# Performance work log

Hardware: AMD Instinct MI355X
Metric: run time of the kernel (lower is better)

Reference implementation:

```python
import jax, jax.numpy as jnp
import numpy as np
from jax import lax

# model dims (must match init_kwargs)
NB, E, G0, G1 = 1, 64, 32, 256          # num_blocks, embed_dim, grid rows, grid cols
DM, DIN, DS, DC, DTR = 2048, 4096, 16, 4, 128  # d_model, d_inner, d_state, d_conv, dt_rank
PS, ST, KD = (2, 16), (2, 16), (31, 31)
B, C, T = 8, 64, 4096


def setup_inputs() -> dict:
    key = jax.random.key(0)
    ks = jax.random.split(key, 4)
    rng = np.random.default_rng(0)

    def w(*s, fan=None):
        fan = fan if fan is not None else s[-1]
        return jnp.asarray((rng.standard_normal(s) / np.sqrt(fan)).astype(np.float32))

    # mamba_ssm-style dt bias init: softplus(bias) ~ Uniform-log in [1e-3, 0.1]
    dt = np.exp(rng.uniform(size=(NB, 2, DIN)) * (np.log(0.1) - np.log(1e-3)) + np.log(1e-3))
    dt = np.clip(dt, 1e-4, None)
    bdt = jnp.asarray((dt + np.log(-np.expm1(-dt))).astype(np.float32))
    A_log = jnp.asarray(np.broadcast_to(np.log(np.arange(1, DS + 1, dtype=np.float32)), (NB, 2, DIN, DS)).copy())

    return {
        'x': jax.random.normal(ks[0], (B, C, T), dtype=jnp.float32),
        'mask': jax.random.uniform(ks[1], (B, C, T)) < 0.5,
        'proj_w': w(E, 1, PS[0], PS[1], fan=PS[0] * PS[1]),
        'proj_b': jnp.zeros((E,), jnp.float32),
        'pos_embed': 0.02 * jax.random.normal(ks[2], (1, G1, DM), dtype=jnp.float32),
        'in_proj_w': w(NB, 2, 2 * DIN, DM, fan=DM),
        'conv_w': w(NB, 2, DIN, DC, fan=DC),
        'conv_b': jnp.zeros((NB, 2, DIN), jnp.float32),
        'x_proj_w': w(NB, 2, DTR + 2 * DS, DIN, fan=DIN),
        'dt_proj_w': w(NB, 2, DIN, DTR, fan=DTR),
        'dt_proj_b': bdt,
        'A_log': A_log,
        'Dp': jnp.ones((NB, 2, DIN), jnp.float32),
        'out_proj_w': w(NB, 2, DM, DIN, fan=DIN),
        'ln_g': jnp.ones((NB, DM), jnp.float32),
        'ln_b': jnp.zeros((NB, DM), jnp.float32),
        'dec_conv_w': w(1, 1, KD[0], KD[1], fan=KD[0] * KD[1]),
        'convT_w': w(E, 1, PS[0], PS[1], fan=E),
        'convT_b': jnp.zeros((1,), jnp.float32),
    }


def _layernorm(x, g, b, eps=1e-5):
    m = jnp.mean(x, -1, keepdims=True)
    v = jnp.var(x, -1, keepdims=True)
    return (x - m) * lax.rsqrt(v + eps) * g + b


def _mamba(h, Win, Wc, bc, Wx, Wdt, bdt, Alog, Dp, Wout):
    # h: [B, L, DM]; faithful port of mamba_ssm Mamba (selective scan reference path)
    xz = jnp.einsum('bld,ed->ble', h, Win)               # [B, L, 2*DIN]
    xc, z = jnp.split(xz, 2, axis=-1)
    xc = xc.swapaxes(1, 2)                               # [B, DIN, L]
    xc = lax.conv_general_dilated(xc, Wc[:, None, :], (1,), ((DC - 1, 0),),
                                  dimension_numbers=('NCH', 'OIH', 'NCH'),
                                  feature_group_count=DIN) + bc[None, :, None]
    u = jax.nn.silu(xc).swapaxes(1, 2)                   # [B, L, DIN]
    x_dbl = jnp.einsum('bld,ed->ble', u, Wx)             # [B, L, DTR+2*DS]
    dt = jax.nn.softplus(jnp.einsum('blr,dr->bld', x_dbl[..., :DTR], Wdt) + bdt)
    Bm = x_dbl[..., DTR:DTR + DS]                        # [B, L, DS]
    Cm = x_dbl[..., DTR + DS:]                           # [B, L, DS]
    A = -jnp.exp(Alog)                                   # [DIN, DS]

    def step(hst, inp):
        dt_t, B_t, C_t, u_t = inp                        # [B,DIN],[B,DS],[B,DS],[B,DIN]
        dA = jnp.exp(dt_t[..., None] * A)                # [B, DIN, DS]
        hst = hst * dA + (dt_t * u_t)[..., None] * B_t[:, None, :]
        return hst, jnp.einsum('bds,bs->bd', hst, C_t)

    h0 = jnp.zeros((h.shape[0], DIN, DS), h.dtype)
    xs = (dt.swapaxes(0, 1), Bm.swapaxes(0, 1), Cm.swapaxes(0, 1), u.swapaxes(0, 1))
    _, ys = lax.scan(step, h0, xs)
    y = ys.swapaxes(0, 1) + u * Dp                       # [B, L, DIN]
    y = y * jax.nn.silu(z)
    return jnp.einsum('bld,ed->ble', y, Wout)            # [B, L, DM]


def _forward(x, mask, proj_w, proj_b, pos_embed, in_proj_w, conv_w, conv_b,
             x_proj_w, dt_proj_w, dt_proj_b, A_log, Dp, out_proj_w,
             ln_g, ln_b, dec_conv_w, convT_w, convT_b):
    xm = jnp.where(mask, 0.0, x)                         # x_masked[mask] = 0
    p = lax.conv_general_dilated(xm[:, None], proj_w, ST, 'VALID',
                                 dimension_numbers=('NCHW', 'OIHW', 'NCHW'))
    p = p + proj_b[None, :, None, None]                  # [B, E, G0, G1]
    h = p.reshape(p.shape[0], E * G0, G1).transpose(0, 2, 1) + pos_embed  # [B, G1, DM]
    for i in range(NB):
        a_f = (in_proj_w[i, 0], conv_w[i, 0], conv_b[i, 0], x_proj_w[i, 0], dt_proj_w[i, 0],
               dt_proj_b[i, 0], A_log[i, 0], Dp[i, 0], out_proj_w[i, 0])
        a_r = (in_proj_w[i, 1], conv_w[i, 1], conv_b[i, 1], x_proj_w[i, 1], dt_proj_w[i, 1],
               dt_proj_b[i, 1], A_log[i, 1], Dp[i, 1], out_proj_w[i, 1])
        o = _mamba(h, *a_f) + jnp.flip(_mamba(jnp.flip(h, 1), *a_r), 1)  # bidirectional add
        h = _layernorm(h + o, ln_g[i], ln_b[i])
    # Decoder
    d = lax.conv_general_dilated(h[:, None], dec_conv_w, (1, 1),
                                 (((KD[0] - 1) // 2,) * 2, ((KD[1] - 1) // 2,) * 2),
                                 dimension_numbers=('NCHW', 'OIHW', 'NCHW'))
    d = d[:, 0].transpose(0, 2, 1).reshape(-1, E, G0, G1)
    # ConvTranspose2d(E->1, k=PS, stride=ST) as lhs-dilated conv with flipped kernel
    wct = jnp.flip(convT_w, (2, 3)).swapaxes(0, 1)       # [1, E, kh, kw]
    rec = lax.conv_general_dilated(d, wct, (1, 1),
                                   ((PS[0] - 1, PS[0] - 1), (PS[1] - 1, PS[1] - 1)),
                                   lhs_dilation=ST,
                                   dimension_numbers=('NCHW', 'OIHW', 'NCHW'))
    rec = rec + convT_b[None, :, None, None]
    return rec[:, 0], x                                  # (x_reconstructed, x_original)


def reference(x, mask, proj_w, proj_b, pos_embed, in_proj_w, conv_w, conv_b,
              x_proj_w, dt_proj_w, dt_proj_b, A_log, Dp, out_proj_w,
              ln_g, ln_b, dec_conv_w, convT_w, convT_b):
    return _forward(x, mask, proj_w, proj_b, pos_embed, in_proj_w, conv_w, conv_b,
                    x_proj_w, dt_proj_w, dt_proj_b, A_log, Dp, out_proj_w,
                    ln_g, ln_b, dec_conv_w, convT_w, convT_b)
```

## Files before the change

kernel.cpp:

```cpp
#include <hip/hip_runtime.h>
#include <hip/hip_bf16.h>
#include <math.h>

typedef unsigned short u16;
typedef __attribute__((ext_vector_type(8))) short bf16x8;
typedef __attribute__((ext_vector_type(4))) float f32x4;

__device__ __forceinline__ float b2f(u16 v) {
  unsigned u = ((unsigned)v) << 16;
  return __builtin_bit_cast(float, u);
}
__device__ __forceinline__ u16 f2b(float f) {
  unsigned u = __builtin_bit_cast(unsigned, f);
  unsigned r = u + 0x7fffu + ((u >> 16) & 1u);
  return (u16)(r >> 16);
}
__device__ __forceinline__ void gload_lds16(const u16* g, u16* l) {
  __builtin_amdgcn_global_load_lds(
      (const __attribute__((address_space(1))) void*)g,
      (__attribute__((address_space(3))) void*)l, 16, 0, 0);
}

__global__ __launch_bounds__(256) void cvt_bf16_k(const float* __restrict__ s,
                                                  u16* __restrict__ d, int n4) {
  int i = blockIdx.x * 256 + threadIdx.x;
  if (i < n4) {
    float4 v = ((const float4*)s)[i];
    ushort4 o;
    o.x = f2b(v.x); o.y = f2b(v.y); o.z = f2b(v.z); o.w = f2b(v.w);
    ((ushort4*)d)[i] = o;
  }
}

__global__ __launch_bounds__(256) void toeplitz_k(
    const float* __restrict__ kw, u16* __restrict__ tb)
{
  int i = blockIdx.x * 256 + threadIdx.x;
  if (i >= 31744) return;
  int k = i & 31, n = (i >> 5) & 15, h = (i >> 9) & 1, ki = i >> 10;
  int t = h * 32 + k - n;
  float v = (t >= 0 && t <= 30) ? kw[ki * 31 + t] : 0.f;
  tb[i] = f2b(v);
}

__global__ __launch_bounds__(256) void patchify_k(
    const float* __restrict__ x, const int* __restrict__ mask,
    const float* __restrict__ pw, const float* __restrict__ pb,
    const float* __restrict__ pos, float* __restrict__ h, u16* __restrict__ hb)
{
  int g1 = blockIdx.x, b = blockIdx.y, tid = threadIdx.x;
  __shared__ float sX[64 * 17];
  __shared__ float sW[2048];
  for (int i = tid; i < 64 * 16; i += 256) {
    int r = i >> 4, c = i & 15;
    int gi = (b * 64 + r) * 4096 + g1 * 16 + c;
    sX[r * 17 + c] = mask[gi] ? 0.f : x[gi];
  }
  for (int i = tid; i < 2048; i += 256) sW[i] = pw[i];
  __syncthreads();
  for (int m = tid; m < 2048; m += 256) {
    int e = m >> 5, g0 = m & 31;
    float acc = pb[e];
    const float* w = &sW[e * 32];
#pragma unroll
    for (int kh = 0; kh < 2; ++kh)
#pragma unroll
      for (int kw = 0; kw < 16; ++kw)
        acc += sX[(2 * g0 + kh) * 17 + kw] * w[kh * 16 + kw];
    float v = acc + pos[g1 * 2048 + m];
    long o = ((long)b * 256 + g1) * 2048 + m;
    h[o] = v;
    hb[o] = f2b(v);
  }
}

__global__ __launch_bounds__(512, 2) void gemm256_k(
    const u16* __restrict__ A0,
    const u16* __restrict__ B0, long bStride,
    u16* __restrict__ C0, long cStride,
    const float* __restrict__ cw,
    const float* __restrict__ cb,
    u16* __restrict__ ub)
{
  constexpr int K = 2048, N = 8192, LDA = 2048;
  __shared__ __align__(16) u16 lds[67584];
  u16* As = lds;
  u16* Bs = lds + 32768;
  const int dir = blockIdx.z;
  const u16* A = A0;
  const u16* B = B0 + (long)dir * bStride;
  u16* C = C0 + (long)dir * cStride;
  const int flip = dir;

  const int tid = threadIdx.x;
  const int wave = tid >> 6, lane = tid & 63;
  const int wr = wave >> 2, wc = wave & 3;
  const int bm = blockIdx.y * 256, bn = blockIdx.x * 256;
  const int lr = lane & 15, lq = lane >> 4;

  f32x4 acc[8][4];
#pragma unroll
  for (int i = 0; i < 8; ++i)
#pragma unroll
    for (int j = 0; j < 4; ++j) acc[i][j] = (f32x4){0.f, 0.f, 0.f, 0.f};

  auto stage = [&](int buf, int kt) {
    int k0 = kt << 6;
#pragma unroll
    for (int hf = 0; hf < 2; ++hf)
#pragma unroll
      for (int j = 0; j < 2; ++j) {
        int g = j * 512 + tid;
        int rl = hf * 128 + (g >> 3);
        int gr = (g & 7) ^ ((g >> 3) & 7);
        int ar = flip ? (bm + 255 - rl) : (bm + rl);
        gload_lds16(A + (long)ar * LDA + k0 + gr * 8,
                    &As[buf * 16384 + hf * 8192 + g * 8]);
        gload_lds16(B + (long)(bn + rl) * K + k0 + gr * 8,
                    &Bs[buf * 16384 + hf * 8192 + g * 8]);
      }
  };

  const int nk = K >> 6;
  stage(0, 0);
  for (int kt = 0; kt < nk; ++kt) {
    __builtin_amdgcn_s_barrier();
    __builtin_amdgcn_sched_barrier(0);
    if (kt + 1 < nk) {
      stage((kt + 1) & 1, kt + 1);
      asm volatile("s_waitcnt vmcnt(16)" ::: "memory");
    } else {
      asm volatile("s_waitcnt vmcnt(0)" ::: "memory");
    }
    __builtin_amdgcn_sched_barrier(0);
    __builtin_amdgcn_s_barrier();
    __builtin_amdgcn_sched_barrier(0);
    const int buf = kt & 1;
#pragma unroll
    for (int h = 0; h < 2; ++h) {
      bf16x8 av[8], bv[4];
#pragma unroll
      for (int i = 0; i < 8; ++i) {
        int row = wr * 128 + i * 16 + lr;
        av[i] = *(const bf16x8*)
            &As[buf * 16384 + ((row * 64 + h * 32 + lq * 8) ^ ((row & 7) << 3))];
      }
#pragma unroll
      for (int j = 0; j < 4; ++j) {
        int row = wc * 64 + j * 16 + lr;
        bv[j] = *(const bf16x8*)
            &Bs[buf * 16384 + ((row * 64 + h * 32 + lq * 8) ^ ((row & 7) << 3))];
      }
      __builtin_amdgcn_s_setprio(1);
#pragma unroll
      for (int i = 0; i < 8; ++i)
#pragma unroll
        for (int j = 0; j < 4; ++j)
          acc[i][j] = __builtin_amdgcn_mfma_f32_16x16x32_bf16(
              av[i], bv[j], acc[i][j], 0, 0, 0);
      __builtin_amdgcn_s_setprio(0);
    }
  }

  if (bn < 4096) {
    __syncthreads();
    u16* tile = lds;
#pragma unroll
    for (int i = 0; i < 8; ++i) {
      int r0 = wr * 128 + i * 16 + lq * 4;
#pragma unroll
      for (int j = 0; j < 4; ++j) {
        int col = wc * 64 + j * 16 + lr;
        f32x4 v = acc[i][j];
#pragma unroll
        for (int r = 0; r < 4; ++r)
          tile[(r0 + r) * 264 + col] = f2b(v[r]);
      }
    }
    __syncthreads();
    const int rgrp = tid >> 5, c8 = tid & 31;
    const int d0 = bn + c8 * 8;
    float wv0[8], wv1[8], wv2[8], wv3[8], cbv[8];
#pragma unroll
    for (int e = 0; e < 8; ++e) {
      const float4 wq = *(const float4*)(cw + ((long)dir * 4096 + d0 + e) * 4);
      wv0[e] = wq.x; wv1[e] = wq.y; wv2[e] = wq.z; wv3[e] = wq.w;
      cbv[e] = cb[dir * 4096 + d0 + e];
    }
    const int l0 = rgrp * 16;
    float w0[8], w1[8], w2[8];
#pragma unroll
    for (int e = 0; e < 8; ++e) { w0[e] = 0.f; w1[e] = 0.f; w2[e] = 0.f; }
    if (rgrp > 0) {
      bf16x8 t0 = *(const bf16x8*)&tile[(l0 - 3) * 264 + c8 * 8];
      bf16x8 t1 = *(const bf16x8*)&tile[(l0 - 2) * 264 + c8 * 8];
      bf16x8 t2 = *(const bf16x8*)&tile[(l0 - 1) * 264 + c8 * 8];
#pragma unroll
      for (int e = 0; e < 8; ++e) {
        w0[e] = b2f((u16)t0[e]); w1[e] = b2f((u16)t1[e]); w2[e] = b2f((u16)t2[e]);
      }
    }
    long ubase = ((long)(dir * 8 + blockIdx.y) * 256 + l0) * 4096 + d0;
#pragma unroll
    for (int l = 0; l < 16; ++l) {
      bf16x8 t = *(const bf16x8*)&tile[(l0 + l) * 264 + c8 * 8];
      float cur[8];
#pragma unroll
      for (int e = 0; e < 8; ++e) cur[e] = b2f((u16)t[e]);
      bf16x8 ov;
#pragma unroll
      for (int e = 0; e < 8; ++e) {
        float a = cbv[e] + wv0[e] * w0[e] + wv1[e] * w1[e] + wv2[e] * w2[e] +
                  wv3[e] * cur[e];
        ov[e] = (short)f2b(a / (1.f + __expf(-a)));
      }
      *(bf16x8*)(ub + ubase + (long)l * 4096) = ov;
#pragma unroll
      for (int e = 0; e < 8; ++e) { w0[e] = w1[e]; w1[e] = w2[e]; w2[e] = cur[e]; }
    }
  } else {
#pragma unroll
    for (int i = 0; i < 8; ++i) {
      int r0 = bm + wr * 128 + i * 16 + lq * 4;
#pragma unroll
      for (int j = 0; j < 4; ++j) {
        int col = bn + wc * 64 + j * 16 + lr;
        f32x4 v = acc[i][j];
#pragma unroll
        for (int r = 0; r < 4; ++r)
          C[(long)(r0 + r) * N + col] = f2b(v[r]);
      }
    }
  }
}

template <int EPI, int F32OUT, int BFOUT>
__global__ __launch_bounds__(256) void mfma_gemm_k(
    const u16* __restrict__ A0, long aStride,
    const u16* __restrict__ B0, long bStride,
    float* __restrict__ C0, long cStride,
    u16* __restrict__ Cb0, long cbStride,
    const float* __restrict__ bias0, int biasStride,
    int N, int K, int lda, int flipDir1)
{
  __shared__ __align__(16) u16 As[2][4096];
  __shared__ __align__(16) u16 Bs[2][4096];
  const int dir = blockIdx.z;
  const u16* A = A0 + (long)dir * aStride;
  const u16* B = B0 + (long)dir * bStride;
  float* C = F32OUT ? (C0 + (long)dir * cStride) : nullptr;
  u16* Cb = BFOUT ? (Cb0 + (long)dir * cbStride) : nullptr;
  const float* bias = (EPI == 1) ? (bias0 + (long)dir * biasStride) : nullptr;
  const int flip = flipDir1 && (dir == 1);

  const int tid = threadIdx.x;
  const int wave = tid >> 6, lane = tid & 63;
  const int wr = wave >> 1, wc = wave & 1;
  const int bm = blockIdx.y * 128, bn = blockIdx.x * 128;
  const int lr = lane & 15, lq = lane >> 4;

  f32x4 acc[4][4];
#pragma unroll
  for (int i = 0; i < 4; ++i)
#pragma unroll
    for (int j = 0; j < 4; ++j) acc[i][j] = (f32x4){0.f, 0.f, 0.f, 0.f};

  const int nk = K >> 5;

  auto stage = [&](int buf, int k0) {
#pragma unroll
    for (int iss = 0; iss < 2; ++iss) {
      int ob = wave * 2048 + iss * 1024 + lane * 16;
      int row = ob >> 6, kb = (ob >> 4) & 3;
      int rg = bm + row;
      rg = flip ? ((rg & ~255) | (255 - (rg & 255))) : rg;
      gload_lds16(A + (long)rg * lda + k0 + kb * 8,
                  &As[buf][wave * 1024 + iss * 512]);
      int rb = bn + row; rb = (rb < N) ? rb : (N - 1);
      gload_lds16(B + (long)rb * K + k0 + kb * 8,
                  &Bs[buf][wave * 1024 + iss * 512]);
    }
  };

  stage(0, 0);
  for (int kt = 0; kt < nk; ++kt) {
    __syncthreads();
    if (kt + 1 < nk) stage((kt + 1) & 1, (kt + 1) << 5);
    const int buf = kt & 1;
    bf16x8 av[4], bv[4];
#pragma unroll
    for (int i = 0; i < 4; ++i)
      av[i] = *(const bf16x8*)&As[buf][(wr * 64 + i * 16 + lr) * 32 + lq * 8];
#pragma unroll
    for (int j = 0; j < 4; ++j)
      bv[j] = *(const bf16x8*)&Bs[buf][(wc * 64 + j * 16 + lr) * 32 + lq * 8];
#pragma unroll
    for (int i = 0; i < 4; ++i)
#pragma unroll
      for (int j = 0; j < 4; ++j)
        acc[i][j] = __builtin_amdgcn_mfma_f32_16x16x32_bf16(av[i], bv[j],
                                                            acc[i][j], 0, 0, 0);
  }

#pragma unroll
  for (int i = 0; i < 4; ++i) {
    int r0 = bm + wr * 64 + i * 16 + lq * 4;
#pragma unroll
    for (int j = 0; j < 4; ++j) {
      int col = bn + wc * 64 + j * 16 + lr;
      if (col < N) {
        f32x4 v = acc[i][j];
#pragma unroll
        for (int r = 0; r < 4; ++r) {
          float xv = v[r];
          if (EPI == 1) {
            xv += bias[col];
            xv = (xv > 20.f) ? xv : log1pf(expf(xv));
          }
          if (F32OUT) C[(long)(r0 + r) * N + col] = xv;
          if (BFOUT) Cb[(long)(r0 + r) * N + col] = f2b(xv);
        }
      }
    }
  }
}

__global__ __launch_bounds__(256) void xdbl_part_k(
    const u16* __restrict__ ubf, const u16* __restrict__ Wxbf,
    float* __restrict__ part)
{
  __shared__ __align__(16) u16 As[2][4096];
  __shared__ __align__(16) u16 Bs[2][4096];
  const int dir = blockIdx.z >> 2, split = blockIdx.z & 3;
  const u16* A = ubf + (long)dir * 2048 * 4096;
  const u16* B = Wxbf + (long)dir * 160 * 4096;
  float* C = part + (long)blockIdx.z * 327680;
  const int tid = threadIdx.x;
  const int wave = tid >> 6, lane = tid & 63;
  const int wr = wave >> 1, wc = wave & 1;
  const int bm = blockIdx.y * 128, bn = blockIdx.x * 128;
  const int lr = lane & 15, lq = lane >> 4;

  f32x4 acc[4][4];
#pragma unroll
  for (int i = 0; i < 4; ++i)
#pragma unroll
    for (int j = 0; j < 4; ++j) acc[i][j] = (f32x4){0.f, 0.f, 0.f, 0.f};

  auto stage = [&](int buf, int k0) {
#pragma unroll
    for (int iss = 0; iss < 2; ++iss) {
      int ob = wave * 2048 + iss * 1024 + lane * 16;
      int row = ob >> 6, kb = (ob >> 4) & 3;
      gload_lds16(A + (long)(bm + row) * 4096 + k0 + kb * 8,
                  &As[buf][wave * 1024 + iss * 512]);
      int rb = bn + row; rb = (rb < 160) ? rb : 159;
      gload_lds16(B + (long)rb * 4096 + k0 + kb * 8,
                  &Bs[buf][wave * 1024 + iss * 512]);
    }
  };

  const int kbase = split << 10;
  stage(0, kbase);
  for (int kt = 0; kt < 32; ++kt) {
    __syncthreads();
    if (kt + 1 < 32) stage((kt + 1) & 1, kbase + ((kt + 1) << 5));
    const int buf = kt & 1;
    bf16x8 av[4], bv[4];
#pragma unroll
    for (int i = 0; i < 4; ++i)
      av[i] = *(const bf16x8*)&As[buf][(wr * 64 + i * 16 + lr) * 32 + lq * 8];
#pragma unroll
    for (int j = 0; j < 4; ++j)
      bv[j] = *(const bf16x8*)&Bs[buf][(wc * 64 + j * 16 + lr) * 32 + lq * 8];
#pragma unroll
    for (int i = 0; i < 4; ++i)
#pragma unroll
      for (int j = 0; j < 4; ++j)
        acc[i][j] = __builtin_amdgcn_mfma_f32_16x16x32_bf16(av[i], bv[j],
                                                            acc[i][j], 0, 0, 0);
  }

#pragma unroll
  for (int i = 0; i < 4; ++i) {
    int r0 = bm + wr * 64 + i * 16 + lq * 4;
#pragma unroll
    for (int j = 0; j < 4; ++j) {
      int col = bn + wc * 64 + j * 16 + lr;
      if (col < 160) {
        f32x4 v = acc[i][j];
#pragma unroll
        for (int r = 0; r < 4; ++r)
          C[(long)(r0 + r) * 160 + col] = v[r];
      }
    }
  }
}

__global__ __launch_bounds__(256) void xdbl_reduce_k(
    const float* __restrict__ part, float* __restrict__ xdbl,
    u16* __restrict__ xdbl_bf)
{
  int i = blockIdx.x * 256 + threadIdx.x;
  if (i >= 655360) return;
  int dir = i / 327680, rem = i - dir * 327680;
  long pb = (long)dir * 4 * 327680 + rem;
  float s = part[pb] + part[pb + 327680] + part[pb + 2 * 327680] +
            part[pb + 3 * 327680];
  xdbl[i] = s;
  xdbl_bf[i] = f2b(s);
}

__global__ __launch_bounds__(256) void scan_a_k(
    const u16* __restrict__ dtbuf, const u16* __restrict__ ubuf,
    const float* __restrict__ xdbl, const float* __restrict__ A_log,
    const float* __restrict__ Dpv, u16* __restrict__ ypre,
    float* __restrict__ stend, float* __restrict__ dtsum)
{
  int blk = blockIdx.x;
  int dtile = blk & 15, c = (blk >> 4) & 7, b = (blk >> 7) & 7, dir = blk >> 10;
  int tid = threadIdx.x;
  int d = dtile * 256 + tid;
  int db = dir * 8 + b;

  __shared__ float sB[32][16], sC[32][16];
  long r160 = (long)db * 256 * 160;
  for (int i = tid; i < 1024; i += 256) {
    int l = i >> 5, s = i & 31;
    float v = xdbl[r160 + (long)(c * 32 + l) * 160 + 128 + s];
    if (s < 16) sB[l][s] = v; else sC[l][s - 16] = v;
  }
  __syncthreads();

  float A[16], st[16];
  const float4* ap = (const float4*)(A_log + ((long)dir * 4096 + d) * 16);
#pragma unroll
  for (int q = 0; q < 4; ++q) {
    float4 t = ap[q];
    A[q * 4 + 0] = -__expf(t.x); A[q * 4 + 1] = -__expf(t.y);
    A[q * 4 + 2] = -__expf(t.z); A[q * 4 + 3] = -__expf(t.w);
  }
#pragma unroll
  for (int s = 0; s < 16; ++s) st[s] = 0.f;
  float Dpd = Dpv[dir * 4096 + d];

  long base = (long)db * 256 * 4096 + (long)c * 32 * 4096 + d;
  float dts = 0.f;
  for (int i = 0; i < 32; ++i) {
    float dtv = b2f(dtbuf[base + (long)i * 4096]);
    float uv  = b2f(ubuf[base + (long)i * 4096]);
    dts += dtv;
    float du = dtv * uv;
    float y = 0.f;
#pragma unroll
    for (int s = 0; s < 16; ++s) {
      st[s] = st[s] * __expf(dtv * A[s]) + du * sB[i][s];
      y += st[s] * sC[i][s];
    }
    ypre[base + (long)i * 4096] = f2b(y + uv * Dpd);
  }
  long eb = ((long)(db * 8 + c) * 4096 + d) * 16;
  float4* ep = (float4*)(stend + eb);
#pragma unroll
  for (int q = 0; q < 4; ++q)
    ep[q] = make_float4(st[q * 4], st[q * 4 + 1], st[q * 4 + 2], st[q * 4 + 3]);
  dtsum[(long)(db * 8 + c) * 4096 + d] = dts;
}

__global__ __launch_bounds__(512) void scan_b_k(
    const u16* __restrict__ dtbuf, const u16* __restrict__ xzbf,
    const float* __restrict__ xdbl, const float* __restrict__ A_log,
    const float* __restrict__ stend, const float* __restrict__ dtsum,
    u16* __restrict__ ybuf)
{
  int blk = blockIdx.x;
  int dtile = blk & 63, b = (blk >> 6) & 7, dir = blk >> 9;
  int tid = threadIdx.x;
  int c = tid >> 6, dd = tid & 63;
  int d0 = dtile * 64, d = d0 + dd;
  int db = dir * 8 + b;

  __shared__ float sEnd[8][64][17];
  __shared__ float sT[8][64];
  __shared__ float sC[256][16];

  long eBase = (long)db * 8 * 65536;
  for (int i = tid; i < 8192; i += 512) {
    int cc = i >> 10, rem = i & 1023, dd2 = rem >> 4, s = rem & 15;
    sEnd[cc][dd2][s] = stend[eBase + (long)cc * 65536 + (long)(d0 + dd2) * 16 + s];
  }
  {
    int cc = tid >> 6, dd2 = tid & 63;
    sT[cc][dd2] = dtsum[(long)(db * 8 + cc) * 4096 + d0 + dd2];
  }
  long r160 = (long)db * 256 * 160;
  for (int i = tid; i < 4096; i += 512) {
    int l = i >> 4, s = i & 15;
    sC[l][s] = xdbl[r160 + (long)l * 160 + 144 + s];
  }
  __syncthreads();

  float A[16];
  const float4* ap = (const float4*)(A_log + ((long)dir * 4096 + d) * 16);
#pragma unroll
  for (int q = 0; q < 4; ++q) {
    float4 t = ap[q];
    A[q * 4 + 0] = -__expf(t.x); A[q * 4 + 1] = -__expf(t.y);
    A[q * 4 + 2] = -__expf(t.z); A[q * 4 + 3] = -__expf(t.w);
  }
  float g[16];
#pragma unroll
  for (int s = 0; s < 16; ++s) g[s] = 0.f;
  for (int j = 0; j < c; ++j) {
    float Tj = sT[j][dd];
#pragma unroll
    for (int s = 0; s < 16; ++s)
      g[s] = g[s] * __expf(A[s] * Tj) + sEnd[j][dd][s];
  }

  long base  = (long)db * 256 * 4096 + (long)c * 32 * 4096 + d;
  long zbase = (long)db * 256 * 8192 + (long)c * 32 * 8192 + 4096 + d;
  float cum = 0.f;
  if (c == 0) {
    for (int i = 0; i < 32; ++i) {
      float yp = b2f(ybuf[base + (long)i * 4096]);
      float zv = b2f(xzbf[zbase + (long)i * 8192]);
      float y = yp * (zv / (1.f + __expf(-zv)));
      ybuf[base + (long)i * 4096] = f2b(y);
    }
  } else {
    for (int i = 0; i < 32; ++i) {
      float dtv = b2f(dtbuf[base + (long)i * 4096]);
      cum += dtv;
      float yp = b2f(ybuf[base + (long)i * 4096]);
      float corr = 0.f;
      const int l = c * 32 + i;
#pragma unroll
      for (int s = 0; s < 16; ++s)
        corr += sC[l][s] * __expf(A[s] * cum) * g[s];
      float zv = b2f(xzbf[zbase + (long)i * 8192]);
      float y = (yp + corr) * (zv / (1.f + __expf(-zv)));
      ybuf[base + (long)i * 4096] = f2b(y);
    }
  }
}

__global__ __launch_bounds__(256) void add_ln_k(
    const float* __restrict__ h, const float* __restrict__ o0,
    const float* __restrict__ o1, const float* __restrict__ g,
    const float* __restrict__ bta, float* __restrict__ h2)
{
  int row = blockIdx.x;
  int b = row >> 8, l = row & 255;
  long base = (long)row * 2048;
  long base1 = ((long)b * 256 + (255 - l)) * 2048;
  int t8 = threadIdx.x * 8;
  float v[8];
  float4 x0 = *(const float4*)(h + base + t8);
  float4 x1 = *(const float4*)(h + base + t8 + 4);
  float4 a0 = *(const float4*)(o0 + base + t8);
  float4 a1 = *(const float4*)(o0 + base + t8 + 4);
  float4 c0 = *(const float4*)(o1 + base1 + t8);
  float4 c1 = *(const float4*)(o1 + base1 + t8 + 4);
  v[0] = x0.x + a0.x + c0.x; v[1] = x0.y + a0.y + c0.y;
  v[2] = x0.z + a0.z + c0.z; v[3] = x0.w + a0.w + c0.w;
  v[4] = x1.x + a1.x + c1.x; v[5] = x1.y + a1.y + c1.y;
  v[6] = x1.z + a1.z + c1.z; v[7] = x1.w + a1.w + c1.w;
  float s = 0.f, ss = 0.f;
#pragma unroll
  for (int j = 0; j < 8; ++j) { s += v[j]; ss += v[j] * v[j]; }
#pragma unroll
  for (int off = 32; off >= 1; off >>= 1) {
    s += __shfl_xor(s, off, 64);
    ss += __shfl_xor(ss, off, 64);
  }
  __shared__ float red[8];
  int wid = threadIdx.x >> 6, lane = threadIdx.x & 63;
  if (lane == 0) { red[wid] = s; red[wid + 4] = ss; }
  __syncthreads();
  if (threadIdx.x == 0) {
    red[0] = red[0] + red[1] + red[2] + red[3];
    red[4] = red[4] + red[5] + red[6] + red[7];
  }
  __syncthreads();
  float mean = red[0] * (1.f / 2048.f);
  float var = red[4] * (1.f / 2048.f) - mean * mean;
  float inv = rsqrtf(var + 1e-5f);
  float o[8];
#pragma unroll
  for (int j = 0; j < 8; ++j)
    o[j] = (v[j] - mean) * inv * g[t8 + j] + bta[t8 + j];
  *(float4*)(h2 + base + t8) = make_float4(o[0], o[1], o[2], o[3]);
  *(float4*)(h2 + base + t8 + 4) = make_float4(o[4], o[5], o[6], o[7]);
}

__global__ __launch_bounds__(256) void dec_conv31_k(
    const float* __restrict__ h2, const u16* __restrict__ tb,
    float* __restrict__ dc)
{
  __shared__ __align__(16) u16 sIn[94 * 120];
  const int b = blockIdx.z;
  const int l0 = blockIdx.y * 64;
  const int m0 = blockIdx.x * 64;
  const int tid = threadIdx.x;
  const float* src = h2 + (long)b * 256 * 2048;
  for (int i = tid; i < 94 * 112; i += 256) {
    int r = i / 112, c = i - r * 112;
    int gl = l0 + r - 15, gm = m0 + c - 15;
    float v = 0.f;
    if (gl >= 0 && gl < 256 && gm >= 0 && gm < 2048)
      v = src[(long)gl * 2048 + gm];
    sIn[r * 120 + c] = f2b(v);
  }
  __syncthreads();
  const int wave = tid >> 6, lane = tid & 63;
  const int lr = lane & 15, lq = lane >> 4;

  f32x4 acc[4];
#pragma unroll
  for (int s = 0; s < 4; ++s) acc[s] = (f32x4){0.f, 0.f, 0.f, 0.f};

#pragma unroll 1
  for (int ki = 0; ki < 31; ++ki) {
    const u16* arow = &sIn[(wave * 16 + lr + ki) * 120];
#pragma unroll
    for (int h = 0; h < 2; ++h) {
      bf16x8 bv = *(const bf16x8*)&tb[((ki * 2 + h) * 16 + lr) * 32 + lq * 8];
#pragma unroll
      for (int ms = 0; ms < 4; ++ms) {
        bf16x8 av = *(const bf16x8*)&arow[ms * 16 + h * 32 + lq * 8];
        acc[ms] = __builtin_amdgcn_mfma_f32_16x16x32_bf16(av, bv, acc[ms], 0, 0, 0);
      }
    }
  }
#pragma unroll
  for (int ms = 0; ms < 4; ++ms) {
    f32x4 v = acc[ms];
#pragma unroll
    for (int r = 0; r < 4; ++r)
      dc[((long)b * 256 + l0 + wave * 16 + lq * 4 + r) * 2048 + m0 + ms * 16 + lr]
          = v[r];
  }
}

__global__ __launch_bounds__(256) void convT_k(
    const float* __restrict__ dc, const float* __restrict__ w,
    const float* __restrict__ wb, float* __restrict__ out)
{
  int j = blockIdx.x, b = blockIdx.y;
  __shared__ float sD[2048];
  __shared__ float sW[2048];
  int tid = threadIdx.x;
  const float* drow = dc + ((long)b * 256 + j) * 2048;
  for (int i = tid; i < 2048; i += 256) { sD[i] = drow[i]; sW[i] = w[i]; }
  __syncthreads();
  float cb = wb[0];
  int owlo = tid & 15, ohbase = tid >> 4;
#pragma unroll
  for (int q = 0; q < 4; ++q) {
    int oh = ohbase + q * 16;
    int i = oh >> 1, a = oh & 1;
    float acc = cb;
#pragma unroll 8
    for (int e = 0; e < 64; ++e)
      acc += sD[e * 32 + i] * sW[e * 32 + a * 16 + owlo];
    out[((long)b * 64 + oh) * 4096 + j * 16 + owlo] = acc;
  }
}

extern "C" void kernel_launch(void* const* d_in, const int* in_sizes, int n_in,
                              void* d_out, int out_size, void* d_ws, size_t ws_size,
                              hipStream_t stream)
{
  const float* x      = (const float*)d_in[0];
  const int*   mask   = (const int*)d_in[1];
  const float* proj_w = (const float*)d_in[2];
  const float* proj_b = (const float*)d_in[3];
  const float* pos    = (const float*)d_in[4];
  const float* Wip    = (const float*)d_in[5];
  const float* convw  = (const float*)d_in[6];
  const float* convb  = (const float*)d_in[7];
  const float* Wx     = (const float*)d_in[8];
  const float* Wdt    = (const float*)d_in[9];
  const float* bdt    = (const float*)d_in[10];
  const float* Alog   = (const float*)d_in[11];
  const float* Dpv    = (const float*)d_in[12];
  const float* Wout   = (const float*)d_in[13];
  const float* lng    = (const float*)d_in[14];
  const float* lnb    = (const float*)d_in[15];
  const float* dkw    = (const float*)d_in[16];
  const float* ctw    = (const float*)d_in[17];
  const float* ctb    = (const float*)d_in[18];
  float* out = (float*)d_out;

  char* p = (char*)d_ws;
  u16*   xz_bf   = (u16*)p;
  float* ob      = (float*)p;
  p += 67108864;
  u16*   u_bf    = (u16*)p;
  float* dc      = (float*)p;
  p += 33554432;
  u16*   dt_bf   = (u16*)p; p += 67108864;
  float* xdbl    = (float*)p; p += 2621440;
  u16*   xdbl_bf = (u16*)p;  p += 1310720;
  float* h       = (float*)p; p += 16777216;
  u16*   h_bf    = (u16*)p;  p += 8388608;
  float* h2      = (float*)p; p += 16777216;
  u16*   y_bf    = (u16*)p;  p += 33554432;
  u16*   Wpool   = (u16*)p;  p += 67108864;
  u16*   Wx_bf   = (u16*)p;  p += 2621440;
  u16*   Wdt_bf  = (u16*)p;  p += 2097152;
  u16*   tb      = (u16*)p;  p += 65536;

  float* part   = (float*)(Wpool + 16777216);
  float* st_end = (float*)(Wpool + 16777216);
  float* dtsum  = h2;

  cvt_bf16_k<<<32768, 256, 0, stream>>>(Wip, Wpool, 8388608);
  cvt_bf16_k<<<1280, 256, 0, stream>>>(Wx, Wx_bf, 327680);
  cvt_bf16_k<<<1024, 256, 0, stream>>>(Wdt, Wdt_bf, 262144);
  toeplitz_k<<<124, 256, 0, stream>>>(dkw, tb);

  patchify_k<<<dim3(256, 8), 256, 0, stream>>>(x, mask, proj_w, proj_b, pos, h, h_bf);

  gemm256_k<<<dim3(32, 8, 2), 512, 0, stream>>>(
      h_bf, Wpool, (long)8192 * 2048, xz_bf, (long)2048 * 8192,
      convw, convb, u_bf);

  xdbl_part_k<<<dim3(2, 16, 8), 256, 0, stream>>>(u_bf, Wx_bf, part);
  xdbl_reduce_k<<<2560, 256, 0, stream>>>(part, xdbl, xdbl_bf);

  mfma_gemm_k<1, 0, 1><<<dim3(32, 16, 2), 256, 0, stream>>>(
      xdbl_bf, (long)2048 * 160, Wdt_bf, (long)4096 * 128, nullptr, 0L,
      dt_bf, (long)2048 * 4096, bdt, 4096, 4096, 128, 160, 0);

  scan_a_k<<<2048, 256, 0, stream>>>(dt_bf, u_bf, xdbl, Alog, Dpv, y_bf, st_end, dtsum);
  scan_b_k<<<1024, 512, 0, stream>>>(dt_bf, xz_bf, xdbl, Alog, st_end, dtsum, y_bf);

  cvt_bf16_k<<<16384, 256, 0, stream>>>(Wout, Wpool, 4194304);

  mfma_gemm_k<0, 1, 0><<<dim3(16, 16, 2), 256, 0, stream>>>(
      y_bf, (long)2048 * 4096, Wpool, (long)2048 * 4096, ob, (long)2048 * 2048,
      nullptr, 0L, nullptr, 0, 2048, 4096, 4096, 0);

  add_ln_k<<<2048, 256, 0, stream>>>(h, ob, ob + (long)2048 * 2048, lng, lnb, h2);

  dec_conv31_k<<<dim3(32, 4, 8), 256, 0, stream>>>(h2, tb, dc);

  convT_k<<<dim3(256, 8), 256, 0, stream>>>(dc, ctw, ctb, out);

  hipMemcpyAsync(out + 2097152, x, (size_t)2097152 * 4,
                 hipMemcpyDeviceToDevice, stream);
}
```

Measured before the change: 636.6 us.

## Halve gemm256 K-tile and LDS footprint, split conv epilogue into two halves

The 256x256 GEMM tile now stages a K-slice of 32 instead of 64, with a new XOR swizzle for the 32-wide rows, which halves LDS use. Launch bounds are raised to request 4 blocks per CU. The fused conv+SiLU epilogue no longer needs a full 256-row tile in LDS: it writes one wave-row half at a time and carries the 3-row halo through a small side buffer. The aim is higher occupancy for better latency hiding, at the cost of twice as many barrier iterations, less MFMA work per barrier, and heavy register pressure under the tighter launch bound (128 accumulator floats per thread).

```diff
diff --git a/kernel.cpp b/kernel.cpp
--- a/kernel.cpp
+++ b/kernel.cpp
@@ -74,7 +74,7 @@
   }
 }
 
-__global__ __launch_bounds__(512, 2) void gemm256_k(
+__global__ __launch_bounds__(512, 4) void gemm256_k(
     const u16* __restrict__ A0,
     const u16* __restrict__ B0, long bStride,
     u16* __restrict__ C0, long cStride,
@@ -83,9 +83,9 @@
     u16* __restrict__ ub)
 {
   constexpr int K = 2048, N = 8192, LDA = 2048;
-  __shared__ __align__(16) u16 lds[67584];
+  __shared__ __align__(16) u16 lds[34584];
   u16* As = lds;
-  u16* Bs = lds + 32768;
+  u16* Bs = lds + 16384;
   const int dir = blockIdx.z;
   const u16* A = A0;
   const u16* B = B0 + (long)dir * bStride;
@@ -105,30 +105,27 @@
     for (int j = 0; j < 4; ++j) acc[i][j] = (f32x4){0.f, 0.f, 0.f, 0.f};
 
   auto stage = [&](int buf, int kt) {
-    int k0 = kt << 6;
-#pragma unroll
-    for (int hf = 0; hf < 2; ++hf)
-#pragma unroll
-      for (int j = 0; j < 2; ++j) {
-        int g = j * 512 + tid;
-        int rl = hf * 128 + (g >> 3);
-        int gr = (g & 7) ^ ((g >> 3) & 7);
-        int ar = flip ? (bm + 255 - rl) : (bm + rl);
-        gload_lds16(A + (long)ar * LDA + k0 + gr * 8,
-                    &As[buf * 16384 + hf * 8192 + g * 8]);
-        gload_lds16(B + (long)(bn + rl) * K + k0 + gr * 8,
-                    &Bs[buf * 16384 + hf * 8192 + g * 8]);
-      }
+    int k0 = kt << 5;
+#pragma unroll
+    for (int j = 0; j < 2; ++j) {
+      int g = j * 512 + tid;
+      int row = g >> 2, sp = g & 3;
+      int ss = sp ^ (row & 3) ^ (((row >> 2) & 1) << 1);
+      int ar = flip ? (bm + 255 - row) : (bm + row);
+      gload_lds16(A + (long)ar * LDA + k0 + ss * 8, &As[buf * 8192 + g * 8]);
+      gload_lds16(B + (long)(bn + row) * K + k0 + ss * 8,
+                  &Bs[buf * 8192 + g * 8]);
+    }
   };
 
-  const int nk = K >> 6;
+  const int nk = K >> 5;
   stage(0, 0);
   for (int kt = 0; kt < nk; ++kt) {
     __builtin_amdgcn_s_barrier();
     __builtin_amdgcn_sched_barrier(0);
     if (kt + 1 < nk) {
       stage((kt + 1) & 1, kt + 1);
-      asm volatile("s_waitcnt vmcnt(16)" ::: "memory");
+      asm volatile("s_waitcnt vmcnt(4)" ::: "memory");
     } else {
       asm volatile("s_waitcnt vmcnt(0)" ::: "memory");
     }
@@ -136,48 +133,32 @@
     __builtin_amdgcn_s_barrier();
     __builtin_amdgcn_sched_barrier(0);
     const int buf = kt & 1;
-#pragma unroll
-    for (int h = 0; h < 2; ++h) {
-      bf16x8 av[8], bv[4];
-#pragma unroll
-      for (int i = 0; i < 8; ++i) {
-        int row = wr * 128 + i * 16 + lr;
-        av[i] = *(const bf16x8*)
-            &As[buf * 16384 + ((row * 64 + h * 32 + lq * 8) ^ ((row & 7) << 3))];
-      }
-#pragma unroll
-      for (int j = 0; j < 4; ++j) {
-        int row = wc * 64 + j * 16 + lr;
-        bv[j] = *(const bf16x8*)
-            &Bs[buf * 16384 + ((row * 64 + h * 32 + lq * 8) ^ ((row & 7) << 3))];
-      }
-      __builtin_amdgcn_s_setprio(1);
-#pragma unroll
-      for (int i = 0; i < 8; ++i)
-#pragma unroll
-        for (int j = 0; j < 4; ++j)
-          acc[i][j] = __builtin_amdgcn_mfma_f32_16x16x32_bf16(
-              av[i], bv[j], acc[i][j], 0, 0, 0);
-      __builtin_amdgcn_s_setprio(0);
-    }
+    bf16x8 av[8], bv[4];
+#pragma unroll
+    for (int i = 0; i < 8; ++i) {
+      int R = wr * 128 + i * 16 + lr;
+      int gp = lq ^ (R & 3) ^ (((R >> 2) & 1) << 1);
+      av[i] = *(const bf16x8*)&As[buf * 8192 + R * 32 + gp * 8];
+    }
+#pragma unroll
+    for (int j = 0; j < 4; ++j) {
+      int R = wc * 64 + j * 16 + lr;
+      int gp = lq ^ (R & 3) ^ (((R >> 2) & 1) << 1);
+      bv[j] = *(const bf16x8*)&Bs[buf * 8192 + R * 32 + gp * 8];
+    }
+    __builtin_amdgcn_s_setprio(1);
+#pragma unroll
+    for (int i = 0; i < 8; ++i)
+#pragma unroll
+      for (int j = 0; j < 4; ++j)
+        acc[i][j] = __builtin_amdgcn_mfma_f32_16x16x32_bf16(
+            av[i], bv[j], acc[i][j], 0, 0, 0);
+    __builtin_amdgcn_s_setprio(0);
   }
 
   if (bn < 4096) {
-    __syncthreads();
     u16* tile = lds;
-#pragma unroll
-    for (int i = 0; i < 8; ++i) {
-      int r0 = wr * 128 + i * 16 + lq * 4;
-#pragma unroll
-      for (int j = 0; j < 4; ++j) {
-        int col = wc * 64 + j * 16 + lr;
-        f32x4 v = acc[i][j];
-#pragma unroll
-        for (int r = 0; r < 4; ++r)
-          tile[(r0 + r) * 264 + col] = f2b(v[r]);
-      }
-    }
-    __syncthreads();
+    u16* side = lds + 33792;
     const int rgrp = tid >> 5, c8 = tid & 31;
     const int d0 = bn + c8 * 8;
     float wv0[8], wv1[8], wv2[8], wv3[8], cbv[8];
@@ -187,37 +168,83 @@
       wv0[e] = wq.x; wv1[e] = wq.y; wv2[e] = wq.z; wv3[e] = wq.w;
       cbv[e] = cb[dir * 4096 + d0 + e];
     }
-    const int l0 = rgrp * 16;
     float w0[8], w1[8], w2[8];
-#pragma unroll
-    for (int e = 0; e < 8; ++e) { w0[e] = 0.f; w1[e] = 0.f; w2[e] = 0.f; }
-    if (rgrp > 0) {
-      bf16x8 t0 = *(const bf16x8*)&tile[(l0 - 3) * 264 + c8 * 8];
-      bf16x8 t1 = *(const bf16x8*)&tile[(l0 - 2) * 264 + c8 * 8];
-      bf16x8 t2 = *(const bf16x8*)&tile[(l0 - 1) * 264 + c8 * 8];
-#pragma unroll
-      for (int e = 0; e < 8; ++e) {
-        w0[e] = b2f((u16)t0[e]); w1[e] = b2f((u16)t1[e]); w2[e] = b2f((u16)t2[e]);
+
+    auto writeacc = [&]() {
+#pragma unroll
+      for (int i = 0; i < 8; ++i) {
+        int r0 = i * 16 + lq * 4;
+#pragma unroll
+        for (int j = 0; j < 4; ++j) {
+          int col = wc * 64 + j * 16 + lr;
+          f32x4 v = acc[i][j];
+#pragma unroll
+          for (int r = 0; r < 4; ++r)
+            tile[(r0 + r) * 264 + col] = f2b(v[r]);
+        }
       }
-    }
-    long ubase = ((long)(dir * 8 + blockIdx.y) * 256 + l0) * 4096 + d0;
-#pragma unroll
-    for (int l = 0; l < 16; ++l) {
-      bf16x8 t = *(const bf16x8*)&tile[(l0 + l) * 264 + c8 * 8];
-      float cur[8];
-#pragma unroll
-      for (int e = 0; e < 8; ++e) cur[e] = b2f((u16)t[e]);
-      bf16x8 ov;
-#pragma unroll
-      for (int e = 0; e < 8; ++e) {
-        float a = cbv[e] + wv0[e] * w0[e] + wv1[e] * w1[e] + wv2[e] * w2[e] +
-                  wv3[e] * cur[e];
-        ov[e] = (short)f2b(a / (1.f + __expf(-a)));
+    };
+
+    auto convhalf = [&](int hh) {
+      if (rgrp == 0) {
+        if (hh == 0) {
+#pragma unroll
+          for (int e = 0; e < 8; ++e) { w0[e] = 0.f; w1[e] = 0.f; w2[e] = 0.f; }
+        } else {
+          bf16x8 t0 = *(const bf16x8*)&side[0 * 264 + c8 * 8];
+          bf16x8 t1 = *(const bf16x8*)&side[1 * 264 + c8 * 8];
+          bf16x8 t2 = *(const bf16x8*)&side[2 * 264 + c8 * 8];
+#pragma unroll
+          for (int e = 0; e < 8; ++e) {
+            w0[e] = b2f((u16)t0[e]); w1[e] = b2f((u16)t1[e]);
+            w2[e] = b2f((u16)t2[e]);
+          }
+        }
+      } else {
+        int lb = rgrp * 8;
+        bf16x8 t0 = *(const bf16x8*)&tile[(lb - 3) * 264 + c8 * 8];
+        bf16x8 t1 = *(const bf16x8*)&tile[(lb - 2) * 264 + c8 * 8];
+        bf16x8 t2 = *(const bf16x8*)&tile[(lb - 1) * 264 + c8 * 8];
+#pragma unroll
+        for (int e = 0; e < 8; ++e) {
+          w0[e] = b2f((u16)t0[e]); w1[e] = b2f((u16)t1[e]);
+          w2[e] = b2f((u16)t2[e]);
+        }
       }
-      *(bf16x8*)(ub + ubase + (long)l * 4096) = ov;
-#pragma unroll
-      for (int e = 0; e < 8; ++e) { w0[e] = w1[e]; w1[e] = w2[e]; w2[e] = cur[e]; }
-    }
+      long ubase = ((long)(dir * 8 + blockIdx.y) * 256 + hh * 128 + rgrp * 8)
+                       * 4096 + d0;
+#pragma unroll
+      for (int l = 0; l < 8; ++l) {
+        bf16x8 t = *(const bf16x8*)&tile[(rgrp * 8 + l) * 264 + c8 * 8];
+        float cur[8];
+#pragma unroll
+        for (int e = 0; e < 8; ++e) cur[e] = b2f((u16)t[e]);
+        bf16x8 ov;
+#pragma unroll
+        for (int e = 0; e < 8; ++e) {
+          float a = cbv[e] + wv0[e] * w0[e] + wv1[e] * w1[e] + wv2[e] * w2[e] +
+                    wv3[e] * cur[e];
+          ov[e] = (short)f2b(a / (1.f + __expf(-a)));
+        }
+        *(bf16x8*)(ub + ubase + (long)l * 4096) = ov;
+#pragma unroll
+        for (int e = 0; e < 8; ++e) { w0[e] = w1[e]; w1[e] = w2[e]; w2[e] = cur[e]; }
+      }
+    };
+
+    __syncthreads();
+    if (wr == 0) writeacc();
+    __syncthreads();
+    convhalf(0);
+    if (tid < 96) {
+      int rr = tid >> 5, cc = tid & 31;
+      *(bf16x8*)&side[rr * 264 + cc * 8] =
+          *(const bf16x8*)&tile[(125 + rr) * 264 + cc * 8];
+    }
+    __syncthreads();
+    if (wr == 1) writeacc();
+    __syncthreads();
+    convhalf(1);
   } else {
 #pragma unroll
     for (int i = 0; i < 8; ++i) {
```

Measured after the change: 1.869 ms. 2.94x slower.

## Use 256x256 split-K MFMA GEMM with reduction for output projection

Applied to the files above, without the earlier changes.

Replaces the generic 128-tile MFMA GEMM for the out_proj (2x 2048x2048x4096) with a 512-thread 256x256 tile kernel that uses swizzled LDS and global_load_lds double buffering. K is split in two to get 256 blocks, and a separate kernel sums the two fp32 partials. The goal is higher arithmetic intensity and better CU fill, at the cost of extra fp32 partial traffic (about 64MB written and read) and one more launch.

```diff
diff --git a/kernel.cpp b/kernel.cpp
--- a/kernel.cpp
+++ b/kernel.cpp
@@ -232,6 +232,117 @@
       }
     }
   }
+}
+
+__global__ __launch_bounds__(512, 2) void gemm256o_k(
+    const u16* __restrict__ Y0,
+    const u16* __restrict__ W0,
+    float* __restrict__ part)
+{
+  constexpr int LDK = 4096;
+  __shared__ __align__(16) u16 lds[65536];
+  u16* As = lds;
+  u16* Bs = lds + 32768;
+  const int dir = blockIdx.z >> 1, split = blockIdx.z & 1;
+  const u16* A = Y0 + (long)dir * 2048 * 4096;
+  const u16* B = W0 + (long)dir * 2048 * 4096;
+  float* C = part + (long)blockIdx.z * 4194304;
+  const int kbase = split << 11;
+
+  const int tid = threadIdx.x;
+  const int wave = tid >> 6, lane = tid & 63;
+  const int wr = wave >> 2, wc = wave & 3;
+  const int bm = blockIdx.y * 256, bn = blockIdx.x * 256;
+  const int lr = lane & 15, lq = lane >> 4;
+
+  f32x4 acc[8][4];
+#pragma unroll
+  for (int i = 0; i < 8; ++i)
+#pragma unroll
+    for (int j = 0; j < 4; ++j) acc[i][j] = (f32x4){0.f, 0.f, 0.f, 0.f};
+
+  auto stage = [&](int buf, int kt) {
+    int k0 = kbase + (kt << 6);
+#pragma unroll
+    for (int hf = 0; hf < 2; ++hf)
+#pragma unroll
+      for (int j = 0; j < 2; ++j) {
+        int g = j * 512 + tid;
+        int rl = hf * 128 + (g >> 3);
+        int gr = (g & 7) ^ ((g >> 3) & 7);
+        gload_lds16(A + (long)(bm + rl) * LDK + k0 + gr * 8,
+                    &As[buf * 16384 + hf * 8192 + g * 8]);
+        gload_lds16(B + (long)(bn + rl) * LDK + k0 + gr * 8,
+                    &Bs[buf * 16384 + hf * 8192 + g * 8]);
+      }
+  };
+
+  const int nk = 32;
+  stage(0, 0);
+  for (int kt = 0; kt < nk; ++kt) {
+    __builtin_amdgcn_s_barrier();
+    __builtin_amdgcn_sched_barrier(0);
+    if (kt + 1 < nk) {
+      stage((kt + 1) & 1, kt + 1);
+      asm volatile("s_waitcnt vmcnt(16)" ::: "memory");
+    } else {
+      asm volatile("s_waitcnt vmcnt(0)" ::: "memory");
+    }
+    __builtin_amdgcn_sched_barrier(0);
+    __builtin_amdgcn_s_barrier();
+    __builtin_amdgcn_sched_barrier(0);
+    const int buf = kt & 1;
+#pragma unroll
+    for (int h = 0; h < 2; ++h) {
+      bf16x8 av[8], bv[4];
+#pragma unroll
+      for (int i = 0; i < 8; ++i) {
+        int row = wr * 128 + i * 16 + lr;
+        av[i] = *(const bf16x8*)
+            &As[buf * 16384 + ((row * 64 + h * 32 + lq * 8) ^ ((row & 7) << 3))];
+      }
+#pragma unroll
+      for (int j = 0; j < 4; ++j) {
+        int row = wc * 64 + j * 16 + lr;
+        bv[j] = *(const bf16x8*)
+            &Bs[buf * 16384 + ((row * 64 + h * 32 + lq * 8) ^ ((row & 7) << 3))];
+      }
+      __builtin_amdgcn_s_setprio(1);
+#pragma unroll
+      for (int i = 0; i < 8; ++i)
+#pragma unroll
+        for (int j = 0; j < 4; ++j)
+          acc[i][j] = __builtin_amdgcn_mfma_f32_16x16x32_bf16(
+              av[i], bv[j], acc[i][j], 0, 0, 0);
+      __builtin_amdgcn_s_setprio(0);
+    }
+  }
+
+#pragma unroll
+  for (int i = 0; i < 8; ++i) {
+    int r0 = bm + wr * 128 + i * 16 + lq * 4;
+#pragma unroll
+    for (int j = 0; j < 4; ++j) {
+      int col = bn + wc * 64 + j * 16 + lr;
+      f32x4 v = acc[i][j];
+#pragma unroll
+      for (int r = 0; r < 4; ++r)
+        C[(long)(r0 + r) * 2048 + col] = v[r];
+    }
+  }
+}
+
+__global__ __launch_bounds__(256) void oproj_reduce_k(
+    const float* __restrict__ part, float* __restrict__ ob)
+{
+  int i = blockIdx.x * 256 + threadIdx.x;
+  if (i >= 2097152) return;
+  int dir = i >> 20, rem = i & 1048575;
+  const float4* p0 = (const float4*)(part + (long)(dir * 2) * 4194304) + rem;
+  const float4* p1 = (const float4*)(part + (long)(dir * 2 + 1) * 4194304) + rem;
+  float4 a = *p0, b = *p1;
+  ((float4*)(ob + (long)dir * 4194304))[rem] =
+      make_float4(a.x + b.x, a.y + b.y, a.z + b.z, a.w + b.w);
 }
 
 template <int EPI, int F32OUT, int BFOUT>
@@ -712,9 +823,10 @@
   u16*   Wdt_bf  = (u16*)p;  p += 2097152;
   u16*   tb      = (u16*)p;  p += 65536;
 
-  float* part   = (float*)(Wpool + 16777216);
-  float* st_end = (float*)(Wpool + 16777216);
-  float* dtsum  = h2;
+  float* part    = (float*)(Wpool + 16777216);
+  float* st_end  = (float*)(Wpool + 16777216);
+  float* dtsum   = h2;
+  float* opart   = (float*)dt_bf;
 
   cvt_bf16_k<<<32768, 256, 0, stream>>>(Wip, Wpool, 8388608);
   cvt_bf16_k<<<1280, 256, 0, stream>>>(Wx, Wx_bf, 327680);
@@ -739,9 +851,8 @@
 
   cvt_bf16_k<<<16384, 256, 0, stream>>>(Wout, Wpool, 4194304);
 
-  mfma_gemm_k<0, 1, 0><<<dim3(16, 16, 2), 256, 0, stream>>>(
-      y_bf, (long)2048 * 4096, Wpool, (long)2048 * 4096, ob, (long)2048 * 2048,
-      nullptr, 0L, nullptr, 0, 2048, 4096, 4096, 0);
+  gemm256o_k<<<dim3(8, 8, 4), 512, 0, stream>>>(y_bf, Wpool, opart);
+  oproj_reduce_k<<<8192, 256, 0, stream>>>(opart, ob);
 
   add_ln_k<<<2048, 256, 0, stream>>>(h, ob, ob + (long)2048 * 2048, lng, lnb, h2);
 
```

Result: faster. 623.9 us (-2.0%).
